# Performance work log

Hardware: AMD Instinct MI355X
Metric: run time of the kernel (lower is better)

The kernel has to match this reference:

```python
import jax, jax.numpy as jnp
import numpy as np

ALPHA = 0.2  # LeakyReLU negative slope


def setup_inputs() -> dict:
    key = jax.random.key(0)
    k1, k2, k3, k4 = jax.random.split(key, 4)
    B, N, in_dim, out_dim, n_heads = 4, 2048, 128, 32, 4
    H = jax.random.normal(k1, (B, N, in_dim), dtype=jnp.float32)
    adj = jax.random.randint(k2, (N, N), 0, 2).astype(jnp.float32)
    # xavier-uniform-like init for params
    limW = np.sqrt(6.0 / (in_dim + out_dim))
    W = jax.random.uniform(k3, (n_heads, in_dim, out_dim), minval=-limW, maxval=limW, dtype=jnp.float32)
    lima = np.sqrt(6.0 / (n_heads + 2 * out_dim))
    a = jax.random.uniform(k4, (n_heads, 2 * out_dim), minval=-lima, maxval=lima, dtype=jnp.float32)
    return {"H": H, "adj": adj, "W": W, "a": a}


def reference(H, adj, W, a):
    B, N, _ = H.shape
    n_heads, _, out_dim = W.shape
    # projected features: (B, H, N, F)
    Ht = jnp.einsum('bni,hio->bhno', H, W)
    # split attention vector: e_ij = leaky_relu(a_src . h_i + a_dst . h_j)
    a_src, a_dst = a[:, :out_dim], a[:, out_dim:]
    src = jnp.einsum('bhnf,hf->bhn', Ht, a_src)  # (B,H,N)
    dst = jnp.einsum('bhnf,hf->bhn', Ht, a_dst)  # (B,H,N)
    e = src[:, :, :, None] + dst[:, :, None, :]  # (B,H,N,N)
    e = jnp.where(e >= 0, e, ALPHA * e)          # leaky_relu
    mask = (adj + jnp.eye(N, dtype=adj.dtype)) != 0  # (N,N) bool, self-loops added
    e = jnp.where(mask[None, None], e, -jnp.inf)
    alpha = jax.nn.softmax(e, axis=-1)           # (B,H,N,N)
    H_new = jnp.einsum('bhnj,bhjf->bhnf', alpha, Ht)
    H_new = jnp.where(H_new > 0, H_new, jnp.expm1(H_new))  # ELU
    # concat heads: (B, N, n_heads*out_dim)
    H_new = jnp.transpose(H_new, (0, 2, 1, 3)).reshape(B, N, n_heads * out_dim)
    return H_new, alpha
```

## Files before the change

### kernel.cpp

```cpp
#include <hip/hip_runtime.h>
#include <hip/hip_bf16.h>
#include <math.h>


typedef float f32x4 __attribute__((ext_vector_type(4)));
typedef short bf16x8 __attribute__((ext_vector_type(8)));
typedef unsigned int u32;

#define LRELU 0.2f
#define LOG2E 1.44269504088896f
#define EXP2(x) __builtin_amdgcn_exp2f(x)

__global__ __launch_bounds__(256) void k0_adjI(const float* __restrict__ adj,
                                               unsigned char* __restrict__ adjI) {
    int idx = blockIdx.x * 256 + threadIdx.x;
    int e0 = idx * 4;
    int row = e0 >> 11;
    int c0 = e0 & 2047;
    float4 v = *(const float4*)(adj + (size_t)e0);
    uchar4 o;
    o.x = (v.x != 0.f || c0     == row) ? 1 : 0;
    o.y = (v.y != 0.f || c0 + 1 == row) ? 1 : 0;
    o.z = (v.z != 0.f || c0 + 2 == row) ? 1 : 0;
    o.w = (v.w != 0.f || c0 + 3 == row) ? 1 : 0;
    *(uchar4*)(adjI + (size_t)e0) = o;
}

__global__ __launch_bounds__(256) void k1_ht(const float* __restrict__ H,
                                             const float* __restrict__ W,
                                             const float* __restrict__ a,
                                             __hip_bfloat16* __restrict__ HtT,
                                             float* __restrict__ src,
                                             float* __restrict__ dst) {
    __shared__ float Ws[128 * 32];
    __shared__ float Hs[8 * 128];
    __shared__ float T[32 * 9];

    int t = threadIdx.x;
    int g0 = blockIdx.x * 8;
    int bh = g0 >> 11;
    int n0 = g0 & 2047;
    int b = bh >> 2, h = bh & 3;

    #pragma unroll
    for (int u = 0; u < 16; ++u) Ws[u * 256 + t] = W[h * 4096 + u * 256 + t];
    #pragma unroll
    for (int u = 0; u < 4; ++u) {
        int s = u * 256 + t;
        int r = s >> 7, i = s & 127;
        Hs[s] = H[(size_t)(b * 2048 + n0 + r) * 128 + i];
    }
    __syncthreads();

    int r = t >> 5, f = t & 31;
    float acc = 0.f;
    #pragma unroll
    for (int i = 0; i < 128; ++i) acc += Hs[r * 128 + i] * Ws[i * 32 + f];

    float sv = acc * a[h * 64 + f];
    float dv = acc * a[h * 64 + 32 + f];
    #pragma unroll
    for (int off = 16; off; off >>= 1) {
        sv += __shfl_xor(sv, off);
        dv += __shfl_xor(dv, off);
    }
    if (f == 0) { src[g0 + r] = sv; dst[g0 + r] = dv; }

    T[f * 9 + r] = acc;
    __syncthreads();
    if (t < 128) {
        int fp = t >> 2, p = t & 3;
        __hip_bfloat162 v2;
        v2.x = __float2bfloat16(T[fp * 9 + 2 * p]);
        v2.y = __float2bfloat16(T[fp * 9 + 2 * p + 1]);
        *(__hip_bfloat162*)&HtT[(size_t)(bh * 32 + fp) * 2048 + n0 + 2 * p] = v2;
    }
}

__global__ __launch_bounds__(256, 4) void k2_fused(const unsigned char* __restrict__ adjI,
                                                   const float* __restrict__ src,
                                                   const float* __restrict__ dst,
                                                   const __hip_bfloat16* __restrict__ HtT,
                                                   float* __restrict__ alpha,
                                                   float* __restrict__ outH) {
    __shared__ float dstS[2048];
    __shared__ float rowL[32], rowSrcS[32];
    __shared__ __align__(16) ushort As[32 * 128];
    __shared__ __align__(16) ushort Bs[32 * 128];

    int t = threadIdx.x;
    int mtile = blockIdx.x;
    int bh    = blockIdx.y;
    int lane = t & 63, w = t >> 6;
    int b = bh >> 2, h = bh & 3;
    int row0 = mtile * 32;

    const float4* dst4g = (const float4*)(dst + bh * 2048);
    #pragma unroll
    for (int u = 0; u < 2; ++u) {
        float4 v = dst4g[u * 256 + t];
        v.x *= LOG2E; v.y *= LOG2E; v.z *= LOG2E; v.w *= LOG2E;
        *(float4*)&dstS[(u * 256 + t) * 4] = v;
    }
    if (t < 32) rowSrcS[t] = src[bh * 2048 + row0 + t] * LOG2E;
    __syncthreads();

    for (int rr = 0; rr < 8; ++rr) {
        int r = w * 8 + rr;
        int gr = row0 + r;
        float sn = rowSrcS[r];
        const uint2* a8 = (const uint2*)(adjI + (size_t)gr * 2048);
        float S = 0.f;
        #pragma unroll
        for (int u = 0; u < 4; ++u) {
            uint2 ab = a8[u * 64 + lane];
            int jb = (u * 64 + lane) * 8;
            float4 dv0 = *(const float4*)&dstS[jb];
            float4 dv1 = *(const float4*)&dstS[jb + 4];
            float dj[8] = {dv0.x, dv0.y, dv0.z, dv0.w, dv1.x, dv1.y, dv1.z, dv1.w};
            #pragma unroll
            for (int q = 0; q < 8; ++q) {
                u32 word = (q < 4) ? ab.x : ab.y;
                float ajf = (float)((word >> (8 * (q & 3))) & 0xffu);
                float ee = sn + dj[q];
                float vm = fmaxf(ee, LRELU * ee);
                S = fmaf(EXP2(vm), ajf, S);
            }
        }
        #pragma unroll
        for (int off = 32; off; off >>= 1) S += __shfl_xor(S, off);
        if (lane == 0) rowL[r] = -__log2f(S);
    }
    __syncthreads();

    f32x4 acc = {0.f, 0.f, 0.f, 0.f};
    int wr = w >> 1, wc = w & 1;
    int l15 = lane & 15, l4 = lane >> 4;
    const ushort* Bbase = (const ushort*)HtT + (size_t)bh * 32 * 2048;
    float* alphaRow = alpha + (size_t)(bh * 2048 + row0) * 2048;

    int sr = t >> 5;
    int sc4 = t & 31;
    int bnr = t >> 4;
    int bc8 = t & 15;

    float snR[4], LR[4];
    #pragma unroll
    for (int u = 0; u < 4; ++u) { snR[u] = rowSrcS[sr + u * 8]; LR[u] = rowL[sr + u * 8]; }

    u32 a32[4]; uint4 bvr[2];
    #pragma unroll
    for (int u = 0; u < 4; ++u)
        a32[u] = *(const u32*)(adjI + (size_t)(row0 + sr + u * 8) * 2048 + sc4 * 4);
    #pragma unroll
    for (int u = 0; u < 2; ++u)
        bvr[u] = *(const uint4*)(Bbase + (size_t)(bnr + u * 16) * 2048 + bc8 * 8);

    for (int kc = 0; kc < 16; ++kc) {
        if (kc) {
            asm volatile("s_waitcnt lgkmcnt(0)" ::: "memory");
            __builtin_amdgcn_s_barrier();
        }
        int jb = kc * 128 + sc4 * 4;
        float4 dv = *(const float4*)&dstS[jb];
        float dj[4] = {dv.x, dv.y, dv.z, dv.w};
        #pragma unroll
        for (int u = 0; u < 4; ++u) {
            int r = sr + u * 8;
            float sn = snR[u], L = LR[u];
            u32 ab = a32[u];
            float o[4];
            #pragma unroll
            for (int q = 0; q < 4; ++q) {
                float ajf = (float)((ab >> (8 * q)) & 0xffu);
                float ee = sn + dj[q];
                float v1 = ee + L;
                float v2 = fmaf(ee, LRELU, L);
                float vm = fmaxf(v1, v2);
                o[q] = EXP2(vm) * ajf;
            }
            f32x4 ov = {o[0], o[1], o[2], o[3]};
            __builtin_nontemporal_store(ov, (f32x4*)(alphaRow + (size_t)r * 2048 + jb));
            u32 lo, hi;
            asm volatile("v_cvt_pk_bf16_f32 %0, %1, %2" : "=v"(lo) : "v"(o[0]), "v"(o[1]));
            asm volatile("v_cvt_pk_bf16_f32 %0, %1, %2" : "=v"(hi) : "v"(o[2]), "v"(o[3]));
            uint2 pk = {lo, hi};
            *(uint2*)&As[(r * 128 + sc4 * 4) ^ ((r & 7) << 3)] = pk;
        }
        #pragma unroll
        for (int u = 0; u < 2; ++u) {
            int nr = bnr + u * 16;
            *(uint4*)&Bs[(nr * 128 + bc8 * 8) ^ ((nr & 7) << 3)] = bvr[u];
        }

        if (kc < 15) {
            int jn = (kc + 1) * 128 + sc4 * 4;
            #pragma unroll
            for (int u = 0; u < 4; ++u)
                a32[u] = *(const u32*)(adjI + (size_t)(row0 + sr + u * 8) * 2048 + jn);
            #pragma unroll
            for (int u = 0; u < 2; ++u)
                bvr[u] = *(const uint4*)(Bbase + (size_t)(bnr + u * 16) * 2048 + (kc + 1) * 128 + bc8 * 8);
        }

        asm volatile("s_waitcnt lgkmcnt(0)" ::: "memory");
        __builtin_amdgcn_s_barrier();

        int arow = wr * 16 + l15;
        int bcol = wc * 16 + l15;
        #pragma unroll
        for (int kk = 0; kk < 4; ++kk) {
            int colk = kk * 32 + l4 * 8;
            bf16x8 avf = *(const bf16x8*)&As[(arow * 128 + colk) ^ ((arow & 7) << 3)];
            bf16x8 bvf = *(const bf16x8*)&Bs[(bcol * 128 + colk) ^ ((bcol & 7) << 3)];
            acc = __builtin_amdgcn_mfma_f32_16x16x32_bf16(avf, bvf, acc, 0, 0, 0);
        }
    }

    #pragma unroll
    for (int q = 0; q < 4; ++q) {
        int node = row0 + wr * 16 + l4 * 4 + q;
        float v = acc[q];
        v = (v > 0.f) ? v : expm1f(v);
        outH[(size_t)(b * 2048 + node) * 128 + h * 32 + wc * 16 + l15] = v;
    }
}

extern "C" void kernel_launch(void* const* d_in, const int* in_sizes, int n_in,
                              void* d_out, int out_size, void* d_ws, size_t ws_size,
                              hipStream_t stream) {
    const float* H   = (const float*)d_in[0];
    const float* adj = (const float*)d_in[1];
    const float* W   = (const float*)d_in[2];
    const float* a   = (const float*)d_in[3];

    float* outH  = (float*)d_out;
    float* alpha = outH + (size_t)4 * 2048 * 128;

    char* ws = (char*)d_ws;
    __hip_bfloat16* HtT = (__hip_bfloat16*)ws;
    float* src = (float*)(ws + 2 * 1024 * 1024);
    float* dst = src + 32768;
    unsigned char* adjI = (unsigned char*)(ws + 2 * 1024 * 1024 + 256 * 1024);

    k0_adjI<<<4096, 256, 0, stream>>>(adj, adjI);
    k1_ht<<<4096, 256, 0, stream>>>(H, W, a, HtT, src, dst);
    k2_fused<<<dim3(64, 16), 256, 0, stream>>>(adjI, src, dst, HtT, alpha, outH);
}
```

Measured before the change: 88.49 us.

## Use MFMA for projection kernel and load B fragments directly in attention loop

The projection kernel k1 now converts W to bf16 in LDS and computes Ht with bf16 MFMA instructions over 64-node tiles, in place of a scalar fp32 dot-product loop over 8-node blocks. The src/dst attention scores are now computed from bf16-input MFMA results instead of fp32 accumulation, which may change accuracy. In the fused attention kernel, the Bs LDS staging buffer is removed and each lane loads its HtT MFMA fragments straight from global memory. The k-loop is also restructured as even/odd double-buffered register prefetch with sched barriers, to overlap global loads with the exp/store stage.

```diff
diff --git a/kernel.cpp b/kernel.cpp
--- a/kernel.cpp
+++ b/kernel.cpp
@@ -10,6 +10,12 @@
 #define LRELU 0.2f
 #define LOG2E 1.44269504088896f
 #define EXP2(x) __builtin_amdgcn_exp2f(x)
+
+__device__ inline ushort f2b(float x) {
+    unsigned int u = __float_as_uint(x);
+    u += 0x7fffu + ((u >> 16) & 1u);
+    return (ushort)(u >> 16);
+}
 
 __global__ __launch_bounds__(256) void k0_adjI(const float* __restrict__ adj,
                                                unsigned char* __restrict__ adjI) {
@@ -32,49 +38,58 @@
                                              __hip_bfloat16* __restrict__ HtT,
                                              float* __restrict__ src,
                                              float* __restrict__ dst) {
-    __shared__ float Ws[128 * 32];
-    __shared__ float Hs[8 * 128];
-    __shared__ float T[32 * 9];
+    __shared__ __align__(16) ushort Wbf[32 * 128];
 
     int t = threadIdx.x;
-    int g0 = blockIdx.x * 8;
-    int bh = g0 >> 11;
-    int n0 = g0 & 2047;
+    int ntile = blockIdx.x;
+    int bh    = blockIdx.y;
     int b = bh >> 2, h = bh & 3;
-
-    #pragma unroll
-    for (int u = 0; u < 16; ++u) Ws[u * 256 + t] = W[h * 4096 + u * 256 + t];
-    #pragma unroll
-    for (int u = 0; u < 4; ++u) {
-        int s = u * 256 + t;
-        int r = s >> 7, i = s & 127;
-        Hs[s] = H[(size_t)(b * 2048 + n0 + r) * 128 + i];
+    int lane = t & 63, w = t >> 6;
+    int l15 = lane & 15, l4 = lane >> 4;
+
+    #pragma unroll
+    for (int u = 0; u < 16; ++u) {
+        int idx = u * 256 + t;
+        int i = idx >> 5, f = idx & 31;
+        Wbf[(f * 128 + i) ^ ((f & 7) << 3)] = f2b(W[h * 4096 + idx]);
     }
     __syncthreads();
 
-    int r = t >> 5, f = t & 31;
-    float acc = 0.f;
-    #pragma unroll
-    for (int i = 0; i < 128; ++i) acc += Hs[r * 128 + i] * Ws[i * 32 + f];
-
-    float sv = acc * a[h * 64 + f];
-    float dv = acc * a[h * 64 + 32 + f];
-    #pragma unroll
-    for (int off = 16; off; off >>= 1) {
-        sv += __shfl_xor(sv, off);
-        dv += __shfl_xor(dv, off);
-    }
-    if (f == 0) { src[g0 + r] = sv; dst[g0 + r] = dv; }
-
-    T[f * 9 + r] = acc;
-    __syncthreads();
-    if (t < 128) {
-        int fp = t >> 2, p = t & 3;
-        __hip_bfloat162 v2;
-        v2.x = __float2bfloat16(T[fp * 9 + 2 * p]);
-        v2.y = __float2bfloat16(T[fp * 9 + 2 * p + 1]);
-        *(__hip_bfloat162*)&HtT[(size_t)(bh * 32 + fp) * 2048 + n0 + 2 * p] = v2;
-    }
+    int n = ntile * 64 + w * 16 + l15;
+    const float* hrow = H + ((size_t)(b * 2048) + n) * 128;
+
+    f32x4 acc0 = {0.f, 0.f, 0.f, 0.f};
+    f32x4 acc1 = {0.f, 0.f, 0.f, 0.f};
+    #pragma unroll
+    for (int kc = 0; kc < 4; ++kc) {
+        int k0 = kc * 32 + l4 * 8;
+        float4 h0 = *(const float4*)(hrow + k0);
+        float4 h1 = *(const float4*)(hrow + k0 + 4);
+        union { u32 u[4]; bf16x8 v; } bu;
+        asm("v_cvt_pk_bf16_f32 %0, %1, %2" : "=v"(bu.u[0]) : "v"(h0.x), "v"(h0.y));
+        asm("v_cvt_pk_bf16_f32 %0, %1, %2" : "=v"(bu.u[1]) : "v"(h0.z), "v"(h0.w));
+        asm("v_cvt_pk_bf16_f32 %0, %1, %2" : "=v"(bu.u[2]) : "v"(h1.x), "v"(h1.y));
+        asm("v_cvt_pk_bf16_f32 %0, %1, %2" : "=v"(bu.u[3]) : "v"(h1.z), "v"(h1.w));
+        bf16x8 bfrag = bu.v;
+        bf16x8 af0 = *(const bf16x8*)&Wbf[(l15 * 128 + kc * 32 + l4 * 8) ^ ((l15 & 7) << 3)];
+        bf16x8 af1 = *(const bf16x8*)&Wbf[((16 + l15) * 128 + kc * 32 + l4 * 8) ^ (((16 + l15) & 7) << 3)];
+        acc0 = __builtin_amdgcn_mfma_f32_16x16x32_bf16(af0, bfrag, acc0, 0, 0, 0);
+        acc1 = __builtin_amdgcn_mfma_f32_16x16x32_bf16(af1, bfrag, acc1, 0, 0, 0);
+    }
+
+    float sv = 0.f, dvv = 0.f;
+    ushort* ht = (ushort*)HtT;
+    #pragma unroll
+    for (int r = 0; r < 4; ++r) {
+        int f0 = l4 * 4 + r;
+        sv  += acc0[r] * a[h * 64 + f0]      + acc1[r] * a[h * 64 + 16 + f0];
+        dvv += acc0[r] * a[h * 64 + 32 + f0] + acc1[r] * a[h * 64 + 48 + f0];
+        ht[(size_t)(bh * 32 + f0) * 2048 + n]      = f2b(acc0[r]);
+        ht[(size_t)(bh * 32 + 16 + f0) * 2048 + n] = f2b(acc1[r]);
+    }
+    sv  += __shfl_xor(sv, 16);  sv  += __shfl_xor(sv, 32);
+    dvv += __shfl_xor(dvv, 16); dvv += __shfl_xor(dvv, 32);
+    if (l4 == 0) { src[bh * 2048 + n] = sv; dst[bh * 2048 + n] = dvv; }
 }
 
 __global__ __launch_bounds__(256, 4) void k2_fused(const unsigned char* __restrict__ adjI,
@@ -86,7 +101,6 @@
     __shared__ float dstS[2048];
     __shared__ float rowL[32], rowSrcS[32];
     __shared__ __align__(16) ushort As[32 * 128];
-    __shared__ __align__(16) ushort Bs[32 * 128];
 
     int t = threadIdx.x;
     int mtile = blockIdx.x;
@@ -136,85 +150,82 @@
     f32x4 acc = {0.f, 0.f, 0.f, 0.f};
     int wr = w >> 1, wc = w & 1;
     int l15 = lane & 15, l4 = lane >> 4;
-    const ushort* Bbase = (const ushort*)HtT + (size_t)bh * 32 * 2048;
+    int arow = wr * 16 + l15;
+    const ushort* Bfp = (const ushort*)HtT + (size_t)(bh * 32 + wc * 16 + l15) * 2048 + l4 * 8;
     float* alphaRow = alpha + (size_t)(bh * 2048 + row0) * 2048;
 
     int sr = t >> 5;
     int sc4 = t & 31;
-    int bnr = t >> 4;
-    int bc8 = t & 15;
 
     float snR[4], LR[4];
     #pragma unroll
     for (int u = 0; u < 4; ++u) { snR[u] = rowSrcS[sr + u * 8]; LR[u] = rowL[sr + u * 8]; }
 
-    u32 a32[4]; uint4 bvr[2];
-    #pragma unroll
-    for (int u = 0; u < 4; ++u)
-        a32[u] = *(const u32*)(adjI + (size_t)(row0 + sr + u * 8) * 2048 + sc4 * 4);
-    #pragma unroll
-    for (int u = 0; u < 2; ++u)
-        bvr[u] = *(const uint4*)(Bbase + (size_t)(bnr + u * 16) * 2048 + bc8 * 8);
-
-    for (int kc = 0; kc < 16; ++kc) {
-        if (kc) {
-            asm volatile("s_waitcnt lgkmcnt(0)" ::: "memory");
-            __builtin_amdgcn_s_barrier();
-        }
-        int jb = kc * 128 + sc4 * 4;
+    auto loadA = [&](int k, u32* ar) {
+        #pragma unroll
+        for (int u = 0; u < 4; ++u)
+            ar[u] = *(const u32*)(adjI + (size_t)(row0 + sr + u * 8) * 2048 + k * 128 + sc4 * 4);
+    };
+    auto loadB = [&](int k, bf16x8* br) {
+        #pragma unroll
+        for (int kk = 0; kk < 4; ++kk)
+            br[kk] = *(const bf16x8*)(Bfp + (size_t)k * 128 + kk * 32);
+    };
+    auto stage = [&](int k, const u32* ar) {
+        int jb = k * 128 + sc4 * 4;
         float4 dv = *(const float4*)&dstS[jb];
         float dj[4] = {dv.x, dv.y, dv.z, dv.w};
         #pragma unroll
         for (int u = 0; u < 4; ++u) {
             int r = sr + u * 8;
             float sn = snR[u], L = LR[u];
-            u32 ab = a32[u];
+            u32 ab = ar[u];
             float o[4];
             #pragma unroll
             for (int q = 0; q < 4; ++q) {
                 float ajf = (float)((ab >> (8 * q)) & 0xffu);
                 float ee = sn + dj[q];
-                float v1 = ee + L;
-                float v2 = fmaf(ee, LRELU, L);
-                float vm = fmaxf(v1, v2);
+                float vm = fmaxf(ee + L, fmaf(ee, LRELU, L));
                 o[q] = EXP2(vm) * ajf;
             }
             f32x4 ov = {o[0], o[1], o[2], o[3]};
             __builtin_nontemporal_store(ov, (f32x4*)(alphaRow + (size_t)r * 2048 + jb));
             u32 lo, hi;
-            asm volatile("v_cvt_pk_bf16_f32 %0, %1, %2" : "=v"(lo) : "v"(o[0]), "v"(o[1]));
-            asm volatile("v_cvt_pk_bf16_f32 %0, %1, %2" : "=v"(hi) : "v"(o[2]), "v"(o[3]));
+            asm("v_cvt_pk_bf16_f32 %0, %1, %2" : "=v"(lo) : "v"(o[0]), "v"(o[1]));
+            asm("v_cvt_pk_bf16_f32 %0, %1, %2" : "=v"(hi) : "v"(o[2]), "v"(o[3]));
             uint2 pk = {lo, hi};
             *(uint2*)&As[(r * 128 + sc4 * 4) ^ ((r & 7) << 3)] = pk;
         }
-        #pragma unroll
-        for (int u = 0; u < 2; ++u) {
-            int nr = bnr + u * 16;
-            *(uint4*)&Bs[(nr * 128 + bc8 * 8) ^ ((nr & 7) << 3)] = bvr[u];
+    };
+    auto mfmaPhase = [&](const bf16x8* br) {
+        #pragma unroll
+        for (int kk = 0; kk < 4; ++kk) {
+            bf16x8 af = *(const bf16x8*)&As[(arow * 128 + kk * 32 + l4 * 8) ^ ((arow & 7) << 3)];
+            acc = __builtin_amdgcn_mfma_f32_16x16x32_bf16(af, br[kk], acc, 0, 0, 0);
         }
-
-        if (kc < 15) {
-            int jn = (kc + 1) * 128 + sc4 * 4;
-            #pragma unroll
-            for (int u = 0; u < 4; ++u)
-                a32[u] = *(const u32*)(adjI + (size_t)(row0 + sr + u * 8) * 2048 + jn);
-            #pragma unroll
-            for (int u = 0; u < 2; ++u)
-                bvr[u] = *(const uint4*)(Bbase + (size_t)(bnr + u * 16) * 2048 + (kc + 1) * 128 + bc8 * 8);
-        }
-
+    };
+
+    u32 aE[4], aO[4];
+    bf16x8 bE[4], bO[4];
+    loadA(0, aE); loadB(0, bE);
+
+    for (int kp = 0; kp < 8; ++kp) {
+        int ke = 2 * kp, ko = 2 * kp + 1;
+        if (ke) { asm volatile("s_waitcnt lgkmcnt(0)" ::: "memory"); __builtin_amdgcn_s_barrier(); }
+        loadA(ko, aO); loadB(ko, bO);
+        __builtin_amdgcn_sched_barrier(0);
+        stage(ke, aE);
         asm volatile("s_waitcnt lgkmcnt(0)" ::: "memory");
         __builtin_amdgcn_s_barrier();
-
-        int arow = wr * 16 + l15;
-        int bcol = wc * 16 + l15;
-        #pragma unroll
-        for (int kk = 0; kk < 4; ++kk) {
-            int colk = kk * 32 + l4 * 8;
-            bf16x8 avf = *(const bf16x8*)&As[(arow * 128 + colk) ^ ((arow & 7) << 3)];
-            bf16x8 bvf = *(const bf16x8*)&Bs[(bcol * 128 + colk) ^ ((bcol & 7) << 3)];
-            acc = __builtin_amdgcn_mfma_f32_16x16x32_bf16(avf, bvf, acc, 0, 0, 0);
-        }
+        mfmaPhase(bE);
+        asm volatile("s_waitcnt lgkmcnt(0)" ::: "memory");
+        __builtin_amdgcn_s_barrier();
+        if (ko + 1 < 16) { loadA(ko + 1, aE); loadB(ko + 1, bE); }
+        __builtin_amdgcn_sched_barrier(0);
+        stage(ko, aO);
+        asm volatile("s_waitcnt lgkmcnt(0)" ::: "memory");
+        __builtin_amdgcn_s_barrier();
+        mfmaPhase(bO);
     }
 
     #pragma unroll
@@ -244,6 +255,6 @@
     unsigned char* adjI = (unsigned char*)(ws + 2 * 1024 * 1024 + 256 * 1024);
 
     k0_adjI<<<4096, 256, 0, stream>>>(adj, adjI);
-    k1_ht<<<4096, 256, 0, stream>>>(H, W, a, HtT, src, dst);
+    k1_ht<<<dim3(32, 16), 256, 0, stream>>>(H, W, a, HtT, src, dst);
     k2_fused<<<dim3(64, 16), 256, 0, stream>>>(adjI, src, dst, HtT, alpha, outH);
 }
```

Measured after the change: 75.56 us. 1.17x faster.
